# Kernel tuning notes

Hardware: AMD Instinct MI355X
Metric: run time of the kernel (lower is better)

Reference implementation:

```python
import jax, jax.numpy as jnp
import numpy as np

N = 4096      # tokens
D = 4096      # input_dim
O = 4096      # output_dim
E = 8         # n_experts
R = 16        # LoRA rank (same for all experts)
K = 2         # top_k
TEMP = 1.0    # temperature
ALPHA = 1.0   # LoRA alpha


def setup_inputs() -> dict:
    key = jax.random.key(0)
    ks = jax.random.split(key, 7)
    std = 1.0 / np.sqrt(R)  # LoRALayer init: randn(input_dim, rank) * 1/sqrt(rank)
    return {
        "x": jax.random.normal(ks[0], (N, D), jnp.float32),
        "linear_w": jax.random.normal(ks[1], (D, O), jnp.float32) * 0.02,  # base nn.Linear weight (stored [in,out])
        "linear_b": jnp.zeros((O,), jnp.float32),
        "lora_A": jax.random.normal(ks[2], (E, D, R), jnp.float32) * std,
        "lora_B": jax.random.normal(ks[3], (E, R, O), jnp.float32) * 0.02,  # torch inits B to 0; randomized for nontrivial test
        "gate_w": jax.random.normal(ks[4], (E + 1, D), jnp.float32) * 0.02,  # E+1 GateLayers, each [D,1]
        "bvv": jax.random.randint(ks[5], (N, E), 0, 2, jnp.int32),  # basis_variant_binary_vector (unused in static gating)
    }


def reference(x, linear_w, linear_b, lora_A, lora_B, gate_w, bvv):
    # base path: nn.Linear
    base = x @ linear_w + linear_b                                   # [N, O]
    # all experts evaluated densely: alpha * (x @ A_e @ B_e), batched as grouped GEMMs
    lora = ALPHA * jnp.einsum("ner,ero->neo",
                              jnp.einsum("nd,edr->ner", x, lora_A),
                              lora_B)                                # [N, E, O]
    outputs = jnp.concatenate([base[:, None, :], lora], axis=1)      # [N, E+1, O]

    # static top-k gating
    logits = x @ gate_w.T                                            # [N, E+1]
    base_logits, lora_logits = logits[:, :1], logits[:, 1:]
    top_vals, top_idx = jax.lax.top_k(lora_logits, K)                # [N, K]
    rows = jnp.arange(x.shape[0])[:, None]
    # torch: zeros.scatter(top_idx, top_vals) -> non-selected experts keep logit 0.0
    lora_sparse = jnp.zeros_like(lora_logits).at[rows, top_idx].set(top_vals)
    gates = jax.nn.softmax(
        jnp.concatenate([base_logits, lora_sparse], axis=-1) / TEMP, axis=-1
    )                                                                # [N, E+1]

    return jnp.sum(outputs * gates[..., None], axis=1)               # [N, O]
```

## Files before the change

### kernel.cpp

```cpp
#include <hip/hip_runtime.h>
#include <hip/hip_bf16.h>
#include <math.h>

constexpr int Ncfg = 4096;
constexpr int Dcfg = 4096;
constexpr int Ocfg = 4096;
constexpr int Ecfg = 8;
constexpr int Rcfg = 16;
constexpr int KD   = Dcfg + Ecfg * Rcfg;
constexpr int NKT  = KD / 64;
constexpr float ALPHA_C = 1.0f;
constexpr double TEMP_C = 1.0;

constexpr size_t BT_OFF = 0;
constexpr size_t AP_OFF = BT_OFF + (size_t)Ocfg * KD * 2;
constexpr size_t AT_OFF = AP_OFF + (size_t)Ncfg * KD * 2;
constexpr size_t G_OFF  = AT_OFF + (size_t)Ecfg * Rcfg * Dcfg * 2;

typedef short bf16x8 __attribute__((ext_vector_type(8)));
typedef float f32x4  __attribute__((ext_vector_type(4)));

__device__ __forceinline__ void async_load16(const __hip_bfloat16* g, __hip_bfloat16* l) {
  __builtin_amdgcn_global_load_lds((__attribute__((address_space(1))) void*)(g),
                                   (__attribute__((address_space(3))) void*)(l), 16, 0, 0);
}

__global__ __launch_bounds__(256) void prep_parallel_kernel(
    const float* __restrict__ x,  const float* __restrict__ gw,
    const float* __restrict__ W,  const float* __restrict__ lB,
    const float* __restrict__ lA,
    float* __restrict__ gates, __hip_bfloat16* __restrict__ Ap,
    __hip_bfloat16* __restrict__ BT, __hip_bfloat16* __restrict__ AT) {
  __shared__ union {
    float tile[64][65];
    float atile[256][17];
  } sm;
  const int bid = blockIdx.x;
  const int tid = threadIdx.x;

  if (bid < 512) {
    const int wave = tid >> 6, lane = tid & 63;
    const int na = bid * 8 + wave * 2, nb = na + 1;
    const float4* xa4 = (const float4*)(x + (size_t)na * Dcfg);
    const float4* xb4 = (const float4*)(x + (size_t)nb * Dcfg);
    const float4* gw4 = (const float4*)gw;
    double accA[9], accB[9];
#pragma unroll
    for (int e = 0; e < 9; e++) { accA[e] = 0.0; accB[e] = 0.0; }
    for (int i = 0; i < 16; i++) {
      int fi = lane + 64 * i;
      float4 xa = xa4[fi], xb = xb4[fi];
#pragma unroll
      for (int e = 0; e < 9; e++) {
        float4 w = gw4[e * 1024 + fi];
        accA[e] += (double)xa.x * (double)w.x + (double)xa.y * (double)w.y +
                   (double)xa.z * (double)w.z + (double)xa.w * (double)w.w;
        accB[e] += (double)xb.x * (double)w.x + (double)xb.y * (double)w.y +
                   (double)xb.z * (double)w.z + (double)xb.w * (double)w.w;
      }
    }
#pragma unroll
    for (int off = 32; off >= 1; off >>= 1) {
#pragma unroll
      for (int e = 0; e < 9; e++) {
        accA[e] += __shfl_xor(accA[e], off, 64);
        accB[e] += __shfl_xor(accB[e], off, 64);
      }
    }
    float g0A_l = 0.f, g0B_l = 0.f;
    if (lane == 0) {
#pragma unroll
      for (int r = 0; r < 2; r++) {
        double lg[9];
#pragma unroll
        for (int e = 0; e < 9; e++) lg[e] = r ? accB[e] : accA[e];
        int i1 = 1;
        for (int e = 2; e <= 8; e++) if (lg[e] > lg[i1]) i1 = e;
        int i2 = -1; double v2 = -1e300;
        for (int e = 1; e <= 8; e++) if (e != i1 && lg[e] > v2) { v2 = lg[e]; i2 = e; }
        double vals[9];
        vals[0] = lg[0];
        for (int e = 1; e <= 8; e++) vals[e] = (e == i1 || e == i2) ? lg[e] : 0.0;
        double mx = vals[0];
        for (int e = 1; e < 9; e++) mx = fmax(mx, vals[e]);
        double se = 0.0, ex[9];
        for (int e = 0; e < 9; e++) { ex[e] = exp((vals[e] - mx) / TEMP_C); se += ex[e]; }
        const int n = r ? nb : na;
        for (int e = 0; e < 9; e++) gates[n * 16 + e] = (float)(ex[e] / se);
        if (r == 0) g0A_l = (float)(ex[0] / se); else g0B_l = (float)(ex[0] / se);
      }
    }
    const float g0A = __shfl(g0A_l, 0, 64);
    const float g0B = __shfl(g0B_l, 0, 64);
    __hip_bfloat16* ara = Ap + (size_t)na * KD;
    __hip_bfloat16* arb = Ap + (size_t)nb * KD;
    for (int i = 0; i < 16; i++) {
      int fi = lane + 64 * i;
      float4 xa = xa4[fi], xb = xb4[fi];
      union { ushort4 u; __hip_bfloat16 h[4]; } p;
      p.h[0] = __float2bfloat16(g0A * xa.x);
      p.h[1] = __float2bfloat16(g0A * xa.y);
      p.h[2] = __float2bfloat16(g0A * xa.z);
      p.h[3] = __float2bfloat16(g0A * xa.w);
      *(ushort4*)(ara + (size_t)fi * 4) = p.u;
      p.h[0] = __float2bfloat16(g0B * xb.x);
      p.h[1] = __float2bfloat16(g0B * xb.y);
      p.h[2] = __float2bfloat16(g0B * xb.z);
      p.h[3] = __float2bfloat16(g0B * xb.w);
      *(ushort4*)(arb + (size_t)fi * 4) = p.u;
    }
  } else if (bid < 4736) {
    const float* src; int r0, c0, dstOff;
    if (bid < 4608) {
      int id = bid - 512;
      src = W; r0 = (id & 63) * 64; c0 = (id >> 6) * 64; dstOff = 0;
    } else {
      int id = bid - 4608;
      src = lB; r0 = (id & 1) * 64; c0 = (id >> 1) * 64; dstOff = Dcfg;
    }
#pragma unroll
    for (int it = 0; it < 4; it++) {
      int flat = it * 256 + tid;
      int i = flat >> 4, f = flat & 15;
      float4 v = *(const float4*)(src + (size_t)(r0 + i) * Ocfg + c0 + 4 * f);
      sm.tile[i][4 * f + 0] = v.x;
      sm.tile[i][4 * f + 1] = v.y;
      sm.tile[i][4 * f + 2] = v.z;
      sm.tile[i][4 * f + 3] = v.w;
    }
    __syncthreads();
#pragma unroll
    for (int it = 0; it < 4; it++) {
      int flat = it * 256 + tid;
      int j = flat >> 4, q = flat & 15;
      union { ushort4 u; __hip_bfloat16 h[4]; } p;
      p.h[0] = __float2bfloat16(sm.tile[4 * q + 0][j]);
      p.h[1] = __float2bfloat16(sm.tile[4 * q + 1][j]);
      p.h[2] = __float2bfloat16(sm.tile[4 * q + 2][j]);
      p.h[3] = __float2bfloat16(sm.tile[4 * q + 3][j]);
      *(ushort4*)(BT + (size_t)(c0 + j) * KD + dstOff + r0 + 4 * q) = p.u;
    }
  } else {
    const int id = bid - 4736;
    const int e = id >> 4, d0 = (id & 15) * 256;
#pragma unroll
    for (int it = 0; it < 16; it++) {
      int idx = it * 256 + tid;
      int d = idx >> 4, rr = idx & 15;
      sm.atile[d][rr] = lA[((size_t)e * Dcfg + d0 + d) * Rcfg + rr];
    }
    __syncthreads();
#pragma unroll
    for (int rr = 0; rr < Rcfg; rr++) {
      AT[((size_t)e * Rcfg + rr) * Dcfg + d0 + tid] = __float2bfloat16(sm.atile[tid][rr]);
    }
  }
}

__global__ __launch_bounds__(512) void lora_t_kernel(
    const float* __restrict__ x, const __hip_bfloat16* __restrict__ AT,
    const float* __restrict__ gates, __hip_bfloat16* __restrict__ Ap) {
  const int n0 = blockIdx.x * 16;
  const int tid = threadIdx.x;
  const int wave = tid >> 6, lane = tid & 63;
  const int m = lane & 15, quad = lane >> 4;
  const int kbase = wave * 512;

  f32x4 acc[8] = {};
  const float* xrow = x + (size_t)(n0 + m) * Dcfg + kbase + quad * 8;
  const __hip_bfloat16* atb = AT + (size_t)m * Dcfg + kbase + quad * 8;
#pragma unroll 2
  for (int kb = 0; kb < 512; kb += 32) {
    float4 x0 = *(const float4*)(xrow + kb);
    float4 x1 = *(const float4*)(xrow + kb + 4);
    union { bf16x8 v; __hip_bfloat16 h[8]; } a;
    a.h[0] = __float2bfloat16(x0.x); a.h[1] = __float2bfloat16(x0.y);
    a.h[2] = __float2bfloat16(x0.z); a.h[3] = __float2bfloat16(x0.w);
    a.h[4] = __float2bfloat16(x1.x); a.h[5] = __float2bfloat16(x1.y);
    a.h[6] = __float2bfloat16(x1.z); a.h[7] = __float2bfloat16(x1.w);
#pragma unroll
    for (int e = 0; e < Ecfg; e++) {
      bf16x8 b = *(const bf16x8*)(atb + (size_t)e * Rcfg * Dcfg + kb);
      acc[e] = __builtin_amdgcn_mfma_f32_16x16x32_bf16(a.v, b, acc[e], 0, 0, 0);
    }
  }
  __shared__ f32x4 red[8][8][64];
#pragma unroll
  for (int e = 0; e < Ecfg; e++) red[wave][e][lane] = acc[e];
  __syncthreads();
  {
    const int e = wave;
    f32x4 s = red[0][e][lane];
#pragma unroll
    for (int w = 1; w < 8; w++) s += red[w][e][lane];
#pragma unroll
    for (int rg = 0; rg < 4; rg++) {
      int nn = n0 + quad * 4 + rg;
      float g = gates[nn * 16 + 1 + e];
      Ap[(size_t)nn * KD + Dcfg + e * Rcfg + m] = __float2bfloat16(ALPHA_C * g * s[rg]);
    }
  }
}

#define STG(gbase, lbase, u, ktile)                                              \
  __builtin_amdgcn_global_load_lds(                                              \
      (__attribute__((address_space(1))) void*)((gbase) + (size_t)(u) * 64 * KD  \
                                                + (size_t)(ktile) * 64),         \
      (__attribute__((address_space(3))) void*)((lbase) + (u) * 8192 + dst),     \
      16, 0, 0)

__global__ __launch_bounds__(512, 2) void gemm_kernel(
    const __hip_bfloat16* __restrict__ Ap, const __hip_bfloat16* __restrict__ BT,
    const float* __restrict__ gates, const float* __restrict__ bias,
    float* __restrict__ out) {
  __shared__ char smem[131072];
  const int tid = threadIdx.x;
  const int m0 = blockIdx.y * 256, n0 = blockIdx.x * 256;
  const int wave = tid >> 6, lane = tid & 63;
  const int wm = wave >> 2, wn = wave & 3;
  const int mr = lane & 15, quad = lane >> 4;

  const int trow = tid >> 3;
  const int cswz = (((tid & 7) ^ ((tid >> 3) & 7)) << 3);
  const __hip_bfloat16* gA = Ap + (size_t)(m0 + trow) * KD + cswz;
  const __hip_bfloat16* gB = BT + (size_t)(n0 + trow) * KD + cswz;
  const int dst = tid << 4;

  const int rswz = (mr & 7) << 4;
  const int arow = (wm * 128 + mr) * 128;
  const int brow = (wn * 64 + mr) * 128;

  f32x4 acc[8][4] = {};

  STG(gA, smem,          0, 0); STG(gA, smem,          1, 0);
  STG(gA, smem,          2, 0); STG(gA, smem,          3, 0);
  STG(gB, smem + 32768,  0, 0); STG(gB, smem + 32768,  1, 0);
  STG(gB, smem + 32768,  2, 0); STG(gB, smem + 32768,  3, 0);
  STG(gA, smem + 65536,  0, 1); STG(gA, smem + 65536,  1, 1);
  STG(gA, smem + 65536,  2, 1); STG(gA, smem + 65536,  3, 1);
  STG(gB, smem + 98304,  0, 1); STG(gB, smem + 98304,  1, 1);
  asm volatile("s_waitcnt vmcnt(6)" ::: "memory");
  __builtin_amdgcn_s_barrier();

  for (int kt = 0; kt < NKT; ++kt) {
    const bool odd = kt & 1;
    const char* At = odd ? (smem + 65536) : smem;
    const char* Bt = odd ? (smem + 98304) : (smem + 32768);
    char* An = odd ? smem : (smem + 65536);
    char* Bn = odd ? (smem + 32768) : (smem + 98304);

    bf16x8 a[4][2], b0r[2][2], b1r[2][2];

#pragma unroll
    for (int i = 0; i < 4; ++i)
#pragma unroll
      for (int kh = 0; kh < 2; ++kh)
        a[i][kh] = *(const bf16x8*)(At + arow + i * 2048 + ((kh * 64 + quad * 16) ^ rswz));
#pragma unroll
    for (int j = 0; j < 2; ++j)
#pragma unroll
      for (int kh = 0; kh < 2; ++kh)
        b0r[j][kh] = *(const bf16x8*)(Bt + brow + j * 2048 + ((kh * 64 + quad * 16) ^ rswz));
    if (kt + 1 < NKT) { STG(gB, Bn, 2, kt + 1); STG(gB, Bn, 3, kt + 1); }
    __builtin_amdgcn_s_barrier();
    asm volatile("s_waitcnt lgkmcnt(0)" ::: "memory");
    __builtin_amdgcn_s_setprio(1);
#pragma unroll
    for (int i = 0; i < 4; ++i)
#pragma unroll
      for (int j = 0; j < 2; ++j)
#pragma unroll
        for (int kh = 0; kh < 2; ++kh)
          acc[i][j] = __builtin_amdgcn_mfma_f32_16x16x32_bf16(a[i][kh], b0r[j][kh], acc[i][j], 0, 0, 0);
    __builtin_amdgcn_s_setprio(0);
    __builtin_amdgcn_s_barrier();

#pragma unroll
    for (int j = 0; j < 2; ++j)
#pragma unroll
      for (int kh = 0; kh < 2; ++kh)
        b1r[j][kh] = *(const bf16x8*)(Bt + brow + (2 + j) * 2048 + ((kh * 64 + quad * 16) ^ rswz));
    __builtin_amdgcn_s_barrier();
    asm volatile("s_waitcnt lgkmcnt(0)" ::: "memory");
    __builtin_amdgcn_s_setprio(1);
#pragma unroll
    for (int i = 0; i < 4; ++i)
#pragma unroll
      for (int j = 0; j < 2; ++j)
#pragma unroll
        for (int kh = 0; kh < 2; ++kh)
          acc[i][2 + j] = __builtin_amdgcn_mfma_f32_16x16x32_bf16(a[i][kh], b1r[j][kh], acc[i][2 + j], 0, 0, 0);
    __builtin_amdgcn_s_setprio(0);
    __builtin_amdgcn_s_barrier();

#pragma unroll
    for (int i = 0; i < 4; ++i)
#pragma unroll
      for (int kh = 0; kh < 2; ++kh)
        a[i][kh] = *(const bf16x8*)(At + arow + (4 + i) * 2048 + ((kh * 64 + quad * 16) ^ rswz));
    __builtin_amdgcn_s_barrier();
    asm volatile("s_waitcnt lgkmcnt(0)" ::: "memory");
    __builtin_amdgcn_s_setprio(1);
#pragma unroll
    for (int i = 0; i < 4; ++i)
#pragma unroll
      for (int j = 0; j < 2; ++j)
#pragma unroll
        for (int kh = 0; kh < 2; ++kh)
          acc[4 + i][2 + j] = __builtin_amdgcn_mfma_f32_16x16x32_bf16(a[i][kh], b1r[j][kh], acc[4 + i][2 + j], 0, 0, 0);
    __builtin_amdgcn_s_setprio(0);
    __builtin_amdgcn_s_barrier();

    if (kt + 2 < NKT) {
      char* Ac = (char*)At; char* Bc = (char*)Bt;
      STG(gA, Ac, 0, kt + 2); STG(gA, Ac, 1, kt + 2);
      STG(gA, Ac, 2, kt + 2); STG(gA, Ac, 3, kt + 2);
      STG(gB, Bc, 0, kt + 2); STG(gB, Bc, 1, kt + 2);
    }
    __builtin_amdgcn_s_setprio(1);
#pragma unroll
    for (int i = 0; i < 4; ++i)
#pragma unroll
      for (int j = 0; j < 2; ++j)
#pragma unroll
        for (int kh = 0; kh < 2; ++kh)
          acc[4 + i][j] = __builtin_amdgcn_mfma_f32_16x16x32_bf16(a[i][kh], b0r[j][kh], acc[4 + i][j], 0, 0, 0);
    __builtin_amdgcn_s_setprio(0);
    if (kt + 2 < NKT) {
      asm volatile("s_waitcnt vmcnt(6)" ::: "memory");
    } else if (kt + 1 < NKT) {
      asm volatile("s_waitcnt vmcnt(0)" ::: "memory");
    }
    if (kt + 1 < NKT) __builtin_amdgcn_s_barrier();
  }

  float bv[4];
#pragma unroll
  for (int j = 0; j < 4; ++j) bv[j] = bias[n0 + wn * 64 + j * 16 + mr];
#pragma unroll
  for (int i = 0; i < 8; ++i) {
    const int rowb = m0 + wm * 128 + i * 16 + quad * 4;
#pragma unroll
    for (int rg = 0; rg < 4; ++rg) {
      const int row = rowb + rg;
      const float g0 = gates[row * 16];
      float* orow = out + (size_t)row * Ocfg + n0 + wn * 64 + mr;
#pragma unroll
      for (int j = 0; j < 4; ++j)
        orow[j * 16] = acc[i][j][rg] + g0 * bv[j];
    }
  }
}

extern "C" void kernel_launch(void* const* d_in, const int* in_sizes, int n_in,
                              void* d_out, int out_size, void* d_ws, size_t ws_size,
                              hipStream_t stream) {
  const float* x  = (const float*)d_in[0];
  const float* W  = (const float*)d_in[1];
  const float* b  = (const float*)d_in[2];
  const float* lA = (const float*)d_in[3];
  const float* lB = (const float*)d_in[4];
  const float* gw = (const float*)d_in[5];
  float* out = (float*)d_out;

  char* ws = (char*)d_ws;
  __hip_bfloat16* BT    = (__hip_bfloat16*)(ws + BT_OFF);
  __hip_bfloat16* Ap    = (__hip_bfloat16*)(ws + AP_OFF);
  __hip_bfloat16* AT    = (__hip_bfloat16*)(ws + AT_OFF);
  float*          gates = (float*)(ws + G_OFF);

  prep_parallel_kernel<<<dim3(4864), 256, 0, stream>>>(x, gw, W, lB, lA, gates, Ap, BT, AT);
  lora_t_kernel<<<dim3(Ncfg / 16), 512, 0, stream>>>(x, AT, gates, Ap);
  gemm_kernel<<<dim3(Ocfg / 256, Ncfg / 256), 512, 0, stream>>>(Ap, BT, gates, b, out);
}
```

Measured before the change: 347.4 us.

## Fuse gate logits and x scaling into the LoRA down-projection kernel

Gate logit computation, softmax gating and the scaled-bf16 conversion of x move out of the prep kernel into the LoRA down-projection kernel, which now reads each x tile once for both the MFMA projection and the double-precision gate dot products. The prep kernel is left to handle only the weight transposes. The aim is to avoid reading x twice from memory and to drop the gate round trip through global memory. The cost is heavier per-thread FP64 work and extra register pressure inside the MFMA loop, plus the loss of its unroll pragma.

```diff
diff --git a/kernel.cpp b/kernel.cpp
--- a/kernel.cpp
+++ b/kernel.cpp
@@ -26,10 +26,8 @@
 }
 
 __global__ __launch_bounds__(256) void prep_parallel_kernel(
-    const float* __restrict__ x,  const float* __restrict__ gw,
     const float* __restrict__ W,  const float* __restrict__ lB,
     const float* __restrict__ lA,
-    float* __restrict__ gates, __hip_bfloat16* __restrict__ Ap,
     __hip_bfloat16* __restrict__ BT, __hip_bfloat16* __restrict__ AT) {
   __shared__ union {
     float tile[64][65];
@@ -38,62 +36,165 @@
   const int bid = blockIdx.x;
   const int tid = threadIdx.x;
 
-  if (bid < 512) {
-    const int wave = tid >> 6, lane = tid & 63;
-    const int na = bid * 8 + wave * 2, nb = na + 1;
-    const float4* xa4 = (const float4*)(x + (size_t)na * Dcfg);
-    const float4* xb4 = (const float4*)(x + (size_t)nb * Dcfg);
-    const float4* gw4 = (const float4*)gw;
-    double accA[9], accB[9];
-#pragma unroll
-    for (int e = 0; e < 9; e++) { accA[e] = 0.0; accB[e] = 0.0; }
-    for (int i = 0; i < 16; i++) {
-      int fi = lane + 64 * i;
-      float4 xa = xa4[fi], xb = xb4[fi];
-#pragma unroll
-      for (int e = 0; e < 9; e++) {
-        float4 w = gw4[e * 1024 + fi];
-        accA[e] += (double)xa.x * (double)w.x + (double)xa.y * (double)w.y +
-                   (double)xa.z * (double)w.z + (double)xa.w * (double)w.w;
-        accB[e] += (double)xb.x * (double)w.x + (double)xb.y * (double)w.y +
-                   (double)xb.z * (double)w.z + (double)xb.w * (double)w.w;
-      }
-    }
-#pragma unroll
-    for (int off = 32; off >= 1; off >>= 1) {
-#pragma unroll
-      for (int e = 0; e < 9; e++) {
-        accA[e] += __shfl_xor(accA[e], off, 64);
-        accB[e] += __shfl_xor(accB[e], off, 64);
-      }
-    }
-    float g0A_l = 0.f, g0B_l = 0.f;
-    if (lane == 0) {
-#pragma unroll
-      for (int r = 0; r < 2; r++) {
-        double lg[9];
-#pragma unroll
-        for (int e = 0; e < 9; e++) lg[e] = r ? accB[e] : accA[e];
-        int i1 = 1;
-        for (int e = 2; e <= 8; e++) if (lg[e] > lg[i1]) i1 = e;
-        int i2 = -1; double v2 = -1e300;
-        for (int e = 1; e <= 8; e++) if (e != i1 && lg[e] > v2) { v2 = lg[e]; i2 = e; }
-        double vals[9];
-        vals[0] = lg[0];
-        for (int e = 1; e <= 8; e++) vals[e] = (e == i1 || e == i2) ? lg[e] : 0.0;
-        double mx = vals[0];
-        for (int e = 1; e < 9; e++) mx = fmax(mx, vals[e]);
-        double se = 0.0, ex[9];
-        for (int e = 0; e < 9; e++) { ex[e] = exp((vals[e] - mx) / TEMP_C); se += ex[e]; }
-        const int n = r ? nb : na;
-        for (int e = 0; e < 9; e++) gates[n * 16 + e] = (float)(ex[e] / se);
-        if (r == 0) g0A_l = (float)(ex[0] / se); else g0B_l = (float)(ex[0] / se);
-      }
-    }
-    const float g0A = __shfl(g0A_l, 0, 64);
-    const float g0B = __shfl(g0B_l, 0, 64);
-    __hip_bfloat16* ara = Ap + (size_t)na * KD;
-    __hip_bfloat16* arb = Ap + (size_t)nb * KD;
+  if (bid < 4224) {
+    const float* src; int r0, c0, dstOff;
+    if (bid < 4096) {
+      int id = bid;
+      src = W; r0 = (id & 63) * 64; c0 = (id >> 6) * 64; dstOff = 0;
+    } else {
+      int id = bid - 4096;
+      src = lB; r0 = (id & 1) * 64; c0 = (id >> 1) * 64; dstOff = Dcfg;
+    }
+#pragma unroll
+    for (int it = 0; it < 4; it++) {
+      int flat = it * 256 + tid;
+      int i = flat >> 4, f = flat & 15;
+      float4 v = *(const float4*)(src + (size_t)(r0 + i) * Ocfg + c0 + 4 * f);
+      sm.tile[i][4 * f + 0] = v.x;
+      sm.tile[i][4 * f + 1] = v.y;
+      sm.tile[i][4 * f + 2] = v.z;
+      sm.tile[i][4 * f + 3] = v.w;
+    }
+    __syncthreads();
+#pragma unroll
+    for (int it = 0; it < 4; it++) {
+      int flat = it * 256 + tid;
+      int j = flat >> 4, q = flat & 15;
+      union { ushort4 u; __hip_bfloat16 h[4]; } p;
+      p.h[0] = __float2bfloat16(sm.tile[4 * q + 0][j]);
+      p.h[1] = __float2bfloat16(sm.tile[4 * q + 1][j]);
+      p.h[2] = __float2bfloat16(sm.tile[4 * q + 2][j]);
+      p.h[3] = __float2bfloat16(sm.tile[4 * q + 3][j]);
+      *(ushort4*)(BT + (size_t)(c0 + j) * KD + dstOff + r0 + 4 * q) = p.u;
+    }
+  } else {
+    const int id = bid - 4224;
+    const int e = id >> 4, d0 = (id & 15) * 256;
+#pragma unroll
+    for (int it = 0; it < 16; it++) {
+      int idx = it * 256 + tid;
+      int d = idx >> 4, rr = idx & 15;
+      sm.atile[d][rr] = lA[((size_t)e * Dcfg + d0 + d) * Rcfg + rr];
+    }
+    __syncthreads();
+#pragma unroll
+    for (int rr = 0; rr < Rcfg; rr++) {
+      AT[((size_t)e * Rcfg + rr) * Dcfg + d0 + tid] = __float2bfloat16(sm.atile[tid][rr]);
+    }
+  }
+}
+
+__global__ __launch_bounds__(512) void gates_lora_kernel(
+    const float* __restrict__ x, const float* __restrict__ gw,
+    const __hip_bfloat16* __restrict__ AT,
+    float* __restrict__ gates, __hip_bfloat16* __restrict__ Ap) {
+  const int n0 = blockIdx.x * 16;
+  const int tid = threadIdx.x;
+  const int wave = tid >> 6, lane = tid & 63;
+  const int m = lane & 15, quad = lane >> 4;
+  const int kbase = wave * 512;
+
+  __shared__ union {
+    double dsum[8][16][9];
+    f32x4  red[8][8][64];
+  } sm;
+  __shared__ float gsm[16][16];
+
+  f32x4 acc[8] = {};
+  double acc9[9];
+#pragma unroll
+  for (int e = 0; e < 9; e++) acc9[e] = 0.0;
+
+  const float* xrow = x + (size_t)(n0 + m) * Dcfg + kbase + quad * 8;
+  const float* gwr  = gw + kbase + quad * 8;
+  const __hip_bfloat16* atb = AT + (size_t)m * Dcfg + kbase + quad * 8;
+
+  for (int kb = 0; kb < 512; kb += 32) {
+    float4 x0 = *(const float4*)(xrow + kb);
+    float4 x1 = *(const float4*)(xrow + kb + 4);
+    union { bf16x8 v; __hip_bfloat16 h[8]; } a;
+    a.h[0] = __float2bfloat16(x0.x); a.h[1] = __float2bfloat16(x0.y);
+    a.h[2] = __float2bfloat16(x0.z); a.h[3] = __float2bfloat16(x0.w);
+    a.h[4] = __float2bfloat16(x1.x); a.h[5] = __float2bfloat16(x1.y);
+    a.h[6] = __float2bfloat16(x1.z); a.h[7] = __float2bfloat16(x1.w);
+#pragma unroll
+    for (int e = 0; e < Ecfg; e++) {
+      bf16x8 b = *(const bf16x8*)(atb + (size_t)e * Rcfg * Dcfg + kb);
+      acc[e] = __builtin_amdgcn_mfma_f32_16x16x32_bf16(a.v, b, acc[e], 0, 0, 0);
+    }
+    double xd[8];
+    xd[0] = (double)x0.x; xd[1] = (double)x0.y; xd[2] = (double)x0.z; xd[3] = (double)x0.w;
+    xd[4] = (double)x1.x; xd[5] = (double)x1.y; xd[6] = (double)x1.z; xd[7] = (double)x1.w;
+#pragma unroll
+    for (int e = 0; e < 9; e++) {
+      float4 g0v = *(const float4*)(gwr + (size_t)e * Dcfg + kb);
+      float4 g1v = *(const float4*)(gwr + (size_t)e * Dcfg + kb + 4);
+      acc9[e] += xd[0] * (double)g0v.x + xd[1] * (double)g0v.y +
+                 xd[2] * (double)g0v.z + xd[3] * (double)g0v.w +
+                 xd[4] * (double)g1v.x + xd[5] * (double)g1v.y +
+                 xd[6] * (double)g1v.z + xd[7] * (double)g1v.w;
+    }
+  }
+#pragma unroll
+  for (int e = 0; e < 9; e++) {
+    acc9[e] += __shfl_xor(acc9[e], 16, 64);
+    acc9[e] += __shfl_xor(acc9[e], 32, 64);
+  }
+  if (lane < 16) {
+#pragma unroll
+    for (int e = 0; e < 9; e++) sm.dsum[wave][lane][e] = acc9[e];
+  }
+  __syncthreads();
+  if (wave == 0 && lane < 16) {
+    double lg[9];
+#pragma unroll
+    for (int e = 0; e < 9; e++) {
+      double s = 0.0;
+#pragma unroll
+      for (int w = 0; w < 8; w++) s += sm.dsum[w][lane][e];
+      lg[e] = s;
+    }
+    int i1 = 1;
+    for (int e = 2; e <= 8; e++) if (lg[e] > lg[i1]) i1 = e;
+    int i2 = -1; double v2 = -1e300;
+    for (int e = 1; e <= 8; e++) if (e != i1 && lg[e] > v2) { v2 = lg[e]; i2 = e; }
+    double vals[9];
+    vals[0] = lg[0];
+    for (int e = 1; e <= 8; e++) vals[e] = (e == i1 || e == i2) ? lg[e] : 0.0;
+    double mx = vals[0];
+    for (int e = 1; e < 9; e++) mx = fmax(mx, vals[e]);
+    double se = 0.0, ex[9];
+    for (int e = 0; e < 9; e++) { ex[e] = exp((vals[e] - mx) / TEMP_C); se += ex[e]; }
+    const int n = n0 + lane;
+    for (int e = 0; e < 9; e++) {
+      float gf = (float)(ex[e] / se);
+      gates[n * 16 + e] = gf;
+      gsm[lane][e] = gf;
+    }
+  }
+  __syncthreads();
+#pragma unroll
+  for (int e = 0; e < Ecfg; e++) sm.red[wave][e][lane] = acc[e];
+  __syncthreads();
+  {
+    const int e = wave;
+    f32x4 s = sm.red[0][e][lane];
+#pragma unroll
+    for (int w = 1; w < 8; w++) s += sm.red[w][e][lane];
+#pragma unroll
+    for (int rg = 0; rg < 4; rg++) {
+      int nn = n0 + quad * 4 + rg;
+      float g = gsm[quad * 4 + rg][1 + e];
+      Ap[(size_t)nn * KD + Dcfg + e * Rcfg + m] = __float2bfloat16(ALPHA_C * g * s[rg]);
+    }
+  }
+  {
+    const int ra = 2 * wave, rb = 2 * wave + 1;
+    const float g0A = gsm[ra][0], g0B = gsm[rb][0];
+    const float4* xa4 = (const float4*)(x + (size_t)(n0 + ra) * Dcfg);
+    const float4* xb4 = (const float4*)(x + (size_t)(n0 + rb) * Dcfg);
+    __hip_bfloat16* ara = Ap + (size_t)(n0 + ra) * KD;
+    __hip_bfloat16* arb = Ap + (size_t)(n0 + rb) * KD;
     for (int i = 0; i < 16; i++) {
       int fi = lane + 64 * i;
       float4 xa = xa4[fi], xb = xb4[fi];
@@ -109,96 +210,6 @@
       p.h[3] = __float2bfloat16(g0B * xb.w);
       *(ushort4*)(arb + (size_t)fi * 4) = p.u;
     }
-  } else if (bid < 4736) {
-    const float* src; int r0, c0, dstOff;
-    if (bid < 4608) {
-      int id = bid - 512;
-      src = W; r0 = (id & 63) * 64; c0 = (id >> 6) * 64; dstOff = 0;
-    } else {
-      int id = bid - 4608;
-      src = lB; r0 = (id & 1) * 64; c0 = (id >> 1) * 64; dstOff = Dcfg;
-    }
-#pragma unroll
-    for (int it = 0; it < 4; it++) {
-      int flat = it * 256 + tid;
-      int i = flat >> 4, f = flat & 15;
-      float4 v = *(const float4*)(src + (size_t)(r0 + i) * Ocfg + c0 + 4 * f);
-      sm.tile[i][4 * f + 0] = v.x;
-      sm.tile[i][4 * f + 1] = v.y;
-      sm.tile[i][4 * f + 2] = v.z;
-      sm.tile[i][4 * f + 3] = v.w;
-    }
-    __syncthreads();
-#pragma unroll
-    for (int it = 0; it < 4; it++) {
-      int flat = it * 256 + tid;
-      int j = flat >> 4, q = flat & 15;
-      union { ushort4 u; __hip_bfloat16 h[4]; } p;
-      p.h[0] = __float2bfloat16(sm.tile[4 * q + 0][j]);
-      p.h[1] = __float2bfloat16(sm.tile[4 * q + 1][j]);
-      p.h[2] = __float2bfloat16(sm.tile[4 * q + 2][j]);
-      p.h[3] = __float2bfloat16(sm.tile[4 * q + 3][j]);
-      *(ushort4*)(BT + (size_t)(c0 + j) * KD + dstOff + r0 + 4 * q) = p.u;
-    }
-  } else {
-    const int id = bid - 4736;
-    const int e = id >> 4, d0 = (id & 15) * 256;
-#pragma unroll
-    for (int it = 0; it < 16; it++) {
-      int idx = it * 256 + tid;
-      int d = idx >> 4, rr = idx & 15;
-      sm.atile[d][rr] = lA[((size_t)e * Dcfg + d0 + d) * Rcfg + rr];
-    }
-    __syncthreads();
-#pragma unroll
-    for (int rr = 0; rr < Rcfg; rr++) {
-      AT[((size_t)e * Rcfg + rr) * Dcfg + d0 + tid] = __float2bfloat16(sm.atile[tid][rr]);
-    }
-  }
-}
-
-__global__ __launch_bounds__(512) void lora_t_kernel(
-    const float* __restrict__ x, const __hip_bfloat16* __restrict__ AT,
-    const float* __restrict__ gates, __hip_bfloat16* __restrict__ Ap) {
-  const int n0 = blockIdx.x * 16;
-  const int tid = threadIdx.x;
-  const int wave = tid >> 6, lane = tid & 63;
-  const int m = lane & 15, quad = lane >> 4;
-  const int kbase = wave * 512;
-
-  f32x4 acc[8] = {};
-  const float* xrow = x + (size_t)(n0 + m) * Dcfg + kbase + quad * 8;
-  const __hip_bfloat16* atb = AT + (size_t)m * Dcfg + kbase + quad * 8;
-#pragma unroll 2
-  for (int kb = 0; kb < 512; kb += 32) {
-    float4 x0 = *(const float4*)(xrow + kb);
-    float4 x1 = *(const float4*)(xrow + kb + 4);
-    union { bf16x8 v; __hip_bfloat16 h[8]; } a;
-    a.h[0] = __float2bfloat16(x0.x); a.h[1] = __float2bfloat16(x0.y);
-    a.h[2] = __float2bfloat16(x0.z); a.h[3] = __float2bfloat16(x0.w);
-    a.h[4] = __float2bfloat16(x1.x); a.h[5] = __float2bfloat16(x1.y);
-    a.h[6] = __float2bfloat16(x1.z); a.h[7] = __float2bfloat16(x1.w);
-#pragma unroll
-    for (int e = 0; e < Ecfg; e++) {
-      bf16x8 b = *(const bf16x8*)(atb + (size_t)e * Rcfg * Dcfg + kb);
-      acc[e] = __builtin_amdgcn_mfma_f32_16x16x32_bf16(a.v, b, acc[e], 0, 0, 0);
-    }
-  }
-  __shared__ f32x4 red[8][8][64];
-#pragma unroll
-  for (int e = 0; e < Ecfg; e++) red[wave][e][lane] = acc[e];
-  __syncthreads();
-  {
-    const int e = wave;
-    f32x4 s = red[0][e][lane];
-#pragma unroll
-    for (int w = 1; w < 8; w++) s += red[w][e][lane];
-#pragma unroll
-    for (int rg = 0; rg < 4; rg++) {
-      int nn = n0 + quad * 4 + rg;
-      float g = gates[nn * 16 + 1 + e];
-      Ap[(size_t)nn * KD + Dcfg + e * Rcfg + m] = __float2bfloat16(ALPHA_C * g * s[rg]);
-    }
   }
 }
 
@@ -369,7 +380,7 @@
   __hip_bfloat16* AT    = (__hip_bfloat16*)(ws + AT_OFF);
   float*          gates = (float*)(ws + G_OFF);
 
-  prep_parallel_kernel<<<dim3(4864), 256, 0, stream>>>(x, gw, W, lB, lA, gates, Ap, BT, AT);
-  lora_t_kernel<<<dim3(Ncfg / 16), 512, 0, stream>>>(x, AT, gates, Ap);
+  prep_parallel_kernel<<<dim3(4352), 256, 0, stream>>>(W, lB, lA, BT, AT);
+  gates_lora_kernel<<<dim3(Ncfg / 16), 512, 0, stream>>>(x, gw, AT, gates, Ap);
   gemm_kernel<<<dim3(Ocfg / 256, Ncfg / 256), 512, 0, stream>>>(Ap, BT, gates, b, out);
 }
```

New measurement: 394.9 us. 1.14x slower.

## Restructure GEMM inner loop into row-slab phases with register double-buffered A fragments

Applied to the files above, without the earlier changes.

The per-k-tile MFMA schedule changes from four quadrant phases separated by workgroup barriers to four row-slab phases. All B fragments are loaded once per tile, and A fragments are double-buffered in registers so each slab's LDS reads overlap the previous slab's MFMAs. Most intermediate s_barriers and lgkmcnt waits go away, leaving one wait, a sched_barrier and a barrier before the next global-to-LDS stage. This cuts synchronization stalls and lets LDS reads overlap compute, at the cost of relying on implicit compiler waits and possibly higher register pressure.

```diff
diff --git a/kernel.cpp b/kernel.cpp
--- a/kernel.cpp
+++ b/kernel.cpp
@@ -246,69 +246,69 @@
     const bool odd = kt & 1;
     const char* At = odd ? (smem + 65536) : smem;
     const char* Bt = odd ? (smem + 98304) : (smem + 32768);
-    char* An = odd ? smem : (smem + 65536);
     char* Bn = odd ? (smem + 32768) : (smem + 98304);
 
-    bf16x8 a[4][2], b0r[2][2], b1r[2][2];
-
-#pragma unroll
-    for (int i = 0; i < 4; ++i)
-#pragma unroll
-      for (int kh = 0; kh < 2; ++kh)
-        a[i][kh] = *(const bf16x8*)(At + arow + i * 2048 + ((kh * 64 + quad * 16) ^ rswz));
-#pragma unroll
-    for (int j = 0; j < 2; ++j)
-#pragma unroll
-      for (int kh = 0; kh < 2; ++kh)
-        b0r[j][kh] = *(const bf16x8*)(Bt + brow + j * 2048 + ((kh * 64 + quad * 16) ^ rswz));
+    bf16x8 b[4][2], aX[2][2], aY[2][2];
+
+#pragma unroll
+    for (int j = 0; j < 4; ++j)
+#pragma unroll
+      for (int kh = 0; kh < 2; ++kh)
+        b[j][kh] = *(const bf16x8*)(Bt + brow + j * 2048 + ((kh * 64 + quad * 16) ^ rswz));
+#pragma unroll
+    for (int i = 0; i < 2; ++i)
+#pragma unroll
+      for (int kh = 0; kh < 2; ++kh)
+        aX[i][kh] = *(const bf16x8*)(At + arow + i * 2048 + ((kh * 64 + quad * 16) ^ rswz));
     if (kt + 1 < NKT) { STG(gB, Bn, 2, kt + 1); STG(gB, Bn, 3, kt + 1); }
-    __builtin_amdgcn_s_barrier();
+#pragma unroll
+    for (int i = 0; i < 2; ++i)
+#pragma unroll
+      for (int kh = 0; kh < 2; ++kh)
+        aY[i][kh] = *(const bf16x8*)(At + arow + (2 + i) * 2048 + ((kh * 64 + quad * 16) ^ rswz));
+
+    __builtin_amdgcn_s_setprio(1);
+#pragma unroll
+    for (int i = 0; i < 2; ++i)
+#pragma unroll
+      for (int j = 0; j < 4; ++j)
+#pragma unroll
+        for (int kh = 0; kh < 2; ++kh)
+          acc[i][j] = __builtin_amdgcn_mfma_f32_16x16x32_bf16(aX[i][kh], b[j][kh], acc[i][j], 0, 0, 0);
+    __builtin_amdgcn_s_setprio(0);
+#pragma unroll
+    for (int i = 0; i < 2; ++i)
+#pragma unroll
+      for (int kh = 0; kh < 2; ++kh)
+        aX[i][kh] = *(const bf16x8*)(At + arow + (4 + i) * 2048 + ((kh * 64 + quad * 16) ^ rswz));
+
+    __builtin_amdgcn_s_setprio(1);
+#pragma unroll
+    for (int i = 0; i < 2; ++i)
+#pragma unroll
+      for (int j = 0; j < 4; ++j)
+#pragma unroll
+        for (int kh = 0; kh < 2; ++kh)
+          acc[2 + i][j] = __builtin_amdgcn_mfma_f32_16x16x32_bf16(aY[i][kh], b[j][kh], acc[2 + i][j], 0, 0, 0);
+    __builtin_amdgcn_s_setprio(0);
+#pragma unroll
+    for (int i = 0; i < 2; ++i)
+#pragma unroll
+      for (int kh = 0; kh < 2; ++kh)
+        aY[i][kh] = *(const bf16x8*)(At + arow + (6 + i) * 2048 + ((kh * 64 + quad * 16) ^ rswz));
+
+    __builtin_amdgcn_s_setprio(1);
+#pragma unroll
+    for (int i = 0; i < 2; ++i)
+#pragma unroll
+      for (int j = 0; j < 4; ++j)
+#pragma unroll
+        for (int kh = 0; kh < 2; ++kh)
+          acc[4 + i][j] = __builtin_amdgcn_mfma_f32_16x16x32_bf16(aX[i][kh], b[j][kh], acc[4 + i][j], 0, 0, 0);
+    __builtin_amdgcn_s_setprio(0);
+
     asm volatile("s_waitcnt lgkmcnt(0)" ::: "memory");
-    __builtin_amdgcn_s_setprio(1);
-#pragma unroll
-    for (int i = 0; i < 4; ++i)
-#pragma unroll
-      for (int j = 0; j < 2; ++j)
-#pragma unroll
-        for (int kh = 0; kh < 2; ++kh)
-          acc[i][j] = __builtin_amdgcn_mfma_f32_16x16x32_bf16(a[i][kh], b0r[j][kh], acc[i][j], 0, 0, 0);
-    __builtin_amdgcn_s_setprio(0);
-    __builtin_amdgcn_s_barrier();
-
-#pragma unroll
-    for (int j = 0; j < 2; ++j)
-#pragma unroll
-      for (int kh = 0; kh < 2; ++kh)
-        b1r[j][kh] = *(const bf16x8*)(Bt + brow + (2 + j) * 2048 + ((kh * 64 + quad * 16) ^ rswz));
-    __builtin_amdgcn_s_barrier();
-    asm volatile("s_waitcnt lgkmcnt(0)" ::: "memory");
-    __builtin_amdgcn_s_setprio(1);
-#pragma unroll
-    for (int i = 0; i < 4; ++i)
-#pragma unroll
-      for (int j = 0; j < 2; ++j)
-#pragma unroll
-        for (int kh = 0; kh < 2; ++kh)
-          acc[i][2 + j] = __builtin_amdgcn_mfma_f32_16x16x32_bf16(a[i][kh], b1r[j][kh], acc[i][2 + j], 0, 0, 0);
-    __builtin_amdgcn_s_setprio(0);
-    __builtin_amdgcn_s_barrier();
-
-#pragma unroll
-    for (int i = 0; i < 4; ++i)
-#pragma unroll
-      for (int kh = 0; kh < 2; ++kh)
-        a[i][kh] = *(const bf16x8*)(At + arow + (4 + i) * 2048 + ((kh * 64 + quad * 16) ^ rswz));
-    __builtin_amdgcn_s_barrier();
-    asm volatile("s_waitcnt lgkmcnt(0)" ::: "memory");
-    __builtin_amdgcn_s_setprio(1);
-#pragma unroll
-    for (int i = 0; i < 4; ++i)
-#pragma unroll
-      for (int j = 0; j < 2; ++j)
-#pragma unroll
-        for (int kh = 0; kh < 2; ++kh)
-          acc[4 + i][2 + j] = __builtin_amdgcn_mfma_f32_16x16x32_bf16(a[i][kh], b1r[j][kh], acc[4 + i][2 + j], 0, 0, 0);
-    __builtin_amdgcn_s_setprio(0);
+    __builtin_amdgcn_sched_barrier(0);
     __builtin_amdgcn_s_barrier();
 
     if (kt + 2 < NKT) {
@@ -319,12 +319,12 @@
     }
     __builtin_amdgcn_s_setprio(1);
 #pragma unroll
-    for (int i = 0; i < 4; ++i)
-#pragma unroll
-      for (int j = 0; j < 2; ++j)
+    for (int i = 0; i < 2; ++i)
+#pragma unroll
+      for (int j = 0; j < 4; ++j)
 #pragma unroll
         for (int kh = 0; kh < 2; ++kh)
-          acc[4 + i][j] = __builtin_amdgcn_mfma_f32_16x16x32_bf16(a[i][kh], b0r[j][kh], acc[4 + i][j], 0, 0, 0);
+          acc[6 + i][j] = __builtin_amdgcn_mfma_f32_16x16x32_bf16(aY[i][kh], b[j][kh], acc[6 + i][j], 0, 0, 0);
     __builtin_amdgcn_s_setprio(0);
     if (kt + 2 < NKT) {
       asm volatile("s_waitcnt vmcnt(6)" ::: "memory");
```

Measured after the change: 348.4 us. No clear change (+0.3%).
